# Performance work log

Hardware: AMD Instinct MI355X
Metric: run time of the kernel (lower is better)

Reference implementation:

```python
import jax, jax.numpy as jnp
import numpy as np

B, T, H = 1024, 256, 128

def _gru(x, Wx, Wh, b):
    # Keras GRU (reset_after=True), gate order z, r, h. x: [B,T,D], b: [2,3H]
    xp = x @ Wx + b[0]                      # [B,T,3H]
    h0 = jnp.zeros((x.shape[0], Wh.shape[0]), x.dtype)
    def step(h, xt):
        hp = h @ Wh + b[1]
        xz, xr, xh = jnp.split(xt, 3, axis=-1)
        hz, hr, hn = jnp.split(hp, 3, axis=-1)
        z = jax.nn.sigmoid(xz + hz)
        r = jax.nn.sigmoid(xr + hr)
        hh = jnp.tanh(xh + r * hn)
        return z * h + (1.0 - z) * hh, None
    h, _ = jax.lax.scan(step, h0, jnp.swapaxes(xp, 0, 1))
    return h                                 # [B,H]

def setup_inputs() -> dict:
    key = jax.random.key(0)
    ks = jax.random.split(key, 32)
    def gp(k, shape, scale=0.05):
        return (jax.random.normal(k, shape, dtype=jnp.float32) * scale)
    inp = {
        "spatial": jax.random.normal(ks[0], (B, T, 2), dtype=jnp.float32),
        "hour_idx": jax.random.randint(ks[1], (B, T), 0, 24, dtype=jnp.int32),
        "week_idx": jax.random.randint(ks[2], (B, T), 0, 7, dtype=jnp.int32),
        "E_time": gp(ks[3], (24, H)),
        "E_week": gp(ks[4], (7, H)),
        # spatial GRU (input dim 2)
        "Ws_x": gp(ks[5], (2, 3 * H)), "Ws_h": gp(ks[6], (H, 3 * H)), "bs": gp(ks[7], (2, 3 * H)),
        # hour temporal GRU (input dim 128)
        "Wh_x": gp(ks[8], (H, 3 * H)), "Wh_h": gp(ks[9], (H, 3 * H)), "bh": gp(ks[10], (2, 3 * H)),
        # week temporal GRU (input dim 128)
        "Ww_x": gp(ks[11], (H, 3 * H)), "Ww_h": gp(ks[12], (H, 3 * H)), "bw": gp(ks[13], (2, 3 * H)),
        # attention Dense(3) over the channel axis of size 3
        "Wa": gp(ks[14], (3, 3)), "ba": gp(ks[15], (3,)),
        # MLP
        "W1": gp(ks[16], (H, 1024)), "b1": gp(ks[17], (1024,)),
        "W2": gp(ks[18], (1024, 512)), "b2": gp(ks[19], (512,)),
        "W3": gp(ks[20], (512, 256)), "b3": gp(ks[21], (256,)),
        "W4": gp(ks[22], (256, H)), "b4": gp(ks[23], (H,)),
        "Wo": gp(ks[24], (H, 1)), "bo": gp(ks[25], (1,)),
    }
    return inp

def reference(spatial, hour_idx, week_idx, E_time, E_week,
              Ws_x, Ws_h, bs, Wh_x, Wh_h, bh, Ww_x, Ww_h, bw,
              Wa, ba, W1, b1, W2, b2, W3, b3, W4, b4, Wo, bo):
    te = E_time[hour_idx]                    # [B,T,128] gather
    we = E_week[week_idx]                    # [B,T,128] gather
    fs = _gru(spatial, Ws_x, Ws_h, bs)       # [B,128]
    fh = _gru(te, Wh_x, Wh_h, bh)            # [B,128]
    fw = _gru(we, Ww_x, Ww_h, bw)            # [B,128]
    allf = jnp.stack([fs, fh, fw], axis=-1)  # [B,128,3]
    scores = jax.nn.softmax(jax.nn.relu(allf @ Wa + ba), axis=-1)
    sf = jnp.sum(allf * scores, axis=-1)     # [B,128] attention-fused features
    x = jax.nn.relu(sf @ W1 + b1)
    x = jax.nn.relu(x @ W2 + b2)
    x = jax.nn.relu(x @ W3 + b3)
    x = jax.nn.relu(x @ W4 + b4)
    out = (x + sf) @ Wo + bo                 # residual then Dense(1)
    return out[:, 0]                         # [B]
```

## Files before the change

### kernel.cpp

```cpp
#include <hip/hip_runtime.h>
#include <hip/hip_bf16.h>

typedef __attribute__((ext_vector_type(8))) short short8;
typedef __attribute__((ext_vector_type(4))) float f32x4;
typedef __attribute__((ext_vector_type(2))) float f32x2;

#define LOG2E  1.44269504088896340736f
#define NLOG2E (-1.44269504088896340736f)
#define TLOG2E (2.88539008177792681472f)

#define HES 168

__device__ __forceinline__ unsigned short f2bf(float f) {
  unsigned u = __builtin_bit_cast(unsigned, f);
  u += 0x7fffu + ((u >> 16) & 1u);
  return (unsigned short)(u >> 16);
}

__global__ __launch_bounds__(256) void ptab_kernel(
    const float* __restrict__ E_time, const float* __restrict__ E_week,
    const float* __restrict__ Wh_x, const float* __restrict__ bh,
    const float* __restrict__ Ww_x, const float* __restrict__ bw,
    float* __restrict__ Ptime, float* __restrict__ Pweek)
{
  const int b = blockIdx.x;
  for (int c = threadIdx.x; c < 384; c += 256) {
    if (b < 24) {
      float acc = bh[c];
      for (int d = 0; d < 128; ++d)
        acc = fmaf(E_time[b * 128 + d], Wh_x[d * 384 + c], acc);
      Ptime[b * 384 + c] = acc;
    } else {
      const int r = b - 24;
      float acc = bw[c];
      for (int d = 0; d < 128; ++d)
        acc = fmaf(E_week[r * 128 + d], Ww_x[d * 384 + c], acc);
      Pweek[r * 384 + c] = acc;
    }
  }
}

__global__ __launch_bounds__(256, 1) void gru_kernel(
    const float* __restrict__ spatial,
    const int* __restrict__ hour_idx,
    const int* __restrict__ week_idx,
    const float* __restrict__ Ws_x,
    const float* __restrict__ Ws_h, const float* __restrict__ bs,
    const float* __restrict__ Wh_h, const float* __restrict__ bh,
    const float* __restrict__ Ww_h, const float* __restrict__ bw,
    const float* __restrict__ Ptime, const float* __restrict__ Pweek,
    const float* __restrict__ W1, const float* __restrict__ W2,
    const float* __restrict__ W3, const float* __restrict__ W4,
    unsigned short* __restrict__ Wt,
    float* __restrict__ fs, float* __restrict__ fh, float* __restrict__ fw)
{
  __shared__ __align__(16) unsigned short hx[2][16 * HES];
  __shared__ float ttile[64][65];

  const int tid = threadIdx.x;

  if (blockIdx.x >= 192) {
    const int tx = tid & 63, ty = tid >> 6;
    for (int t = blockIdx.x - 192; t < 200; t += 64) {
      const float* src; unsigned short* dst; int K, N, tk, tn; int tb = t;
      if (tb < 32)       { src = W1; dst = Wt;          K = 128;  N = 1024; tk = tb >> 4; tn = tb & 15; }
      else if (tb < 160) { tb -= 32;  src = W2; dst = Wt + 131072; K = 1024; N = 512;  tk = tb >> 3; tn = tb & 7; }
      else if (tb < 192) { tb -= 160; src = W3; dst = Wt + 655360; K = 512;  N = 256;  tk = tb >> 2; tn = tb & 3; }
      else               { tb -= 192; src = W4; dst = Wt + 786432; K = 256;  N = 128;  tk = tb >> 1; tn = tb & 1; }
      const int k0 = tk * 64, n0 = tn * 64;
      #pragma unroll
      for (int i = 0; i < 16; ++i)
        ttile[ty * 16 + i][tx] = src[(k0 + ty * 16 + i) * N + n0 + tx];
      __syncthreads();
      #pragma unroll
      for (int i = 0; i < 16; ++i)
        dst[(n0 + ty * 16 + i) * K + k0 + tx] = f2bf(ttile[tx][ty * 16 + i]);
      __syncthreads();
    }
    return;
  }

  const int lane = tid & 63;
  const int wv   = tid >> 6;
  const int ar   = lane & 15;
  const int akg  = lane >> 4;
  const int gid  = blockIdx.x;
  const int gru  = gid >> 6;
  const int row0 = (gid & 63) * 16;

  const float* __restrict__ Wh   = (gru == 0) ? Ws_h : (gru == 1) ? Wh_h : Ww_h;
  const float* __restrict__ bvec = (gru == 0) ? bs   : (gru == 1) ? bh   : bw;
  float* __restrict__ fout       = (gru == 0) ? fs   : (gru == 1) ? fh   : fw;
  const float* __restrict__ Ptab = (gru == 1) ? Ptime : Pweek;
  const int* __restrict__ idxg   = (gru == 1) ? hour_idx : week_idx;
  const int NR = (gru == 1) ? 24 : 7;

  const int jc[2] = {wv * 16 + ar, 64 + wv * 16 + ar};

  short8 wf[2][15];
  #pragma unroll
  for (int jh = 0; jh < 2; ++jh) {
    #pragma unroll
    for (int g = 0; g < 2; ++g) {
      #pragma unroll
      for (int ks = 0; ks < 5; ++ks) {
        short8 f;
        #pragma unroll
        for (int q = 0; q < 8; ++q) {
          const int k = ks * 32 + akg * 8 + q;
          const int col = g * 128 + jc[jh];
          float v;
          if (k < 128) v = Wh[k * 384 + col];
          else {
            const int p = k - 128;
            if (gru == 0) v = (p == 0) ? Ws_x[col] : (p == 1) ? Ws_x[384 + col] : 0.f;
            else          v = (p < NR) ? Ptab[p * 384 + col] : 0.f;
          }
          f[q] = (short)f2bf(v * NLOG2E);
        }
        wf[jh][g * 5 + ks] = f;
      }
    }
    #pragma unroll
    for (int ks = 0; ks < 4; ++ks) {
      short8 f;
      #pragma unroll
      for (int q = 0; q < 8; ++q) {
        const int k = ks * 32 + akg * 8 + q;
        f[q] = (short)f2bf(Wh[k * 384 + 256 + jc[jh]] * TLOG2E);
      }
      wf[jh][10 + ks] = f;
    }
    {
      short8 f;
      #pragma unroll
      for (int q = 0; q < 8; ++q) {
        const int p = akg * 8 + q;
        const int col = 256 + jc[jh];
        float v;
        if (gru == 0) v = (p == 0) ? Ws_x[col] : (p == 1) ? Ws_x[384 + col] : 0.f;
        else          v = (p < NR) ? Ptab[p * 384 + col] : 0.f;
        f[q] = (short)f2bf(v * TLOG2E);
      }
      wf[jh][14] = f;
    }
  }

  float bz[2], br[2], bnh[2], bnx[2];
  #pragma unroll
  for (int jh = 0; jh < 2; ++jh) {
    const int j = jc[jh];
    bz[jh]  = (bvec[384 + j]       + (gru == 0 ? bvec[j]       : 0.f)) * NLOG2E;
    br[jh]  = (bvec[384 + 128 + j] + (gru == 0 ? bvec[128 + j] : 0.f)) * NLOG2E;
    bnh[jh] = bvec[384 + 256 + j] * TLOG2E;
    bnx[jh] = (gru == 0 ? bvec[256 + j] : 0.f) * TLOG2E;
  }

  for (int e = tid; e < 2 * 16 * HES; e += 256) ((unsigned short*)hx)[e] = 0;
  __syncthreads();

  const bool mt  = (tid & 15) == 0;
  const int mrow = tid >> 4;
  f32x2 spn = {0.f, 0.f};
  int ix_prev = 0, ix_cur = 0, ix_next = 0;
  if (mt) {
    if (gru == 0) {
      const f32x2 s0 = *(const f32x2*)&spatial[(row0 + mrow) * 512];
      unsigned pk;
      asm("v_cvt_pk_bf16_f32 %0, %1, %2" : "=v"(pk) : "v"(s0.x), "v"(s0.y));
      *(unsigned*)&hx[0][mrow * HES + 128] = pk;
      spn = *(const f32x2*)&spatial[(row0 + mrow) * 512 + 2];
    } else {
      ix_cur = idxg[(row0 + mrow) * 256];
      hx[0][mrow * HES + 128 + ix_cur] = 0x3F80;
      ix_next = idxg[(row0 + mrow) * 256 + 1];
    }
  }
  __syncthreads();

  float hst[2][4];
  #pragma unroll
  for (int jh = 0; jh < 2; ++jh)
    #pragma unroll
    for (int q = 0; q < 4; ++q) hst[jh][q] = 0.f;

  const int abase = ar * HES;

  for (int t = 0; t < 256; ++t) {
    const unsigned short* __restrict__ hb = hx[t & 1];
    unsigned short* __restrict__ ho       = hx[(t + 1) & 1];

    short8 a[5];
    #pragma unroll
    for (int ks = 0; ks < 5; ++ks)
      a[ks] = *(const short8*)&hb[abase + ks * 32 + akg * 8];

    f32x2 msp = {0.f, 0.f};
    int ixn2 = 0;
    const bool mact = mt && (t + 1 < 256);
    if (mact && gru == 0 && t + 2 < 256)
      msp = *(const f32x2*)&spatial[(row0 + mrow) * 512 + 2 * (t + 2)];
    if (mact && gru != 0 && t + 2 < 256)
      ixn2 = idxg[(row0 + mrow) * 256 + t + 2];

    #pragma unroll
    for (int jh = 0; jh < 2; ++jh) {
      f32x4 az  = {bz[jh],  bz[jh],  bz[jh],  bz[jh]};
      f32x4 arr = {br[jh],  br[jh],  br[jh],  br[jh]};
      f32x4 anh = {bnh[jh], bnh[jh], bnh[jh], bnh[jh]};
      f32x4 anx = {bnx[jh], bnx[jh], bnx[jh], bnx[jh]};
      #pragma unroll
      for (int ks = 0; ks < 4; ++ks) {
        az  = __builtin_amdgcn_mfma_f32_16x16x32_bf16(a[ks], wf[jh][ks],      az,  0, 0, 0);
        arr = __builtin_amdgcn_mfma_f32_16x16x32_bf16(a[ks], wf[jh][5 + ks],  arr, 0, 0, 0);
        anh = __builtin_amdgcn_mfma_f32_16x16x32_bf16(a[ks], wf[jh][10 + ks], anh, 0, 0, 0);
      }
      az  = __builtin_amdgcn_mfma_f32_16x16x32_bf16(a[4], wf[jh][4],  az,  0, 0, 0);
      arr = __builtin_amdgcn_mfma_f32_16x16x32_bf16(a[4], wf[jh][9],  arr, 0, 0, 0);
      anx = __builtin_amdgcn_mfma_f32_16x16x32_bf16(a[4], wf[jh][14], anx, 0, 0, 0);

      float zg[4], rg[4], pz[4], pr[4];
      #pragma unroll
      for (int q = 0; q < 4; ++q) {
        pz[q] = 1.f + __builtin_amdgcn_exp2f(az[q]);
        pr[q] = 1.f + __builtin_amdgcn_exp2f(arr[q]);
      }
      #pragma unroll
      for (int p = 0; p < 4; p += 2) {
        const float A0 = pz[p] * pr[p];
        const float A1 = pz[p + 1] * pr[p + 1];
        const float inv = __builtin_amdgcn_rcpf(A0 * A1);
        const float t1 = A1 * inv, t0 = A0 * inv;
        zg[p]     = pr[p] * t1;     rg[p]     = pz[p] * t1;
        zg[p + 1] = pr[p + 1] * t0; rg[p + 1] = pz[p + 1] * t0;
      }
      float ph[4];
      #pragma unroll
      for (int q = 0; q < 4; ++q)
        ph[q] = 1.f + __builtin_amdgcn_exp2f(fmaf(rg[q], anh[q], anx[q]));
      float hn4[4];
      #pragma unroll
      for (int p = 0; p < 4; p += 2) {
        const float inv = __builtin_amdgcn_rcpf(ph[p] * ph[p + 1]);
        const float i0 = ph[p + 1] * inv;
        const float i1 = ph[p] * inv;
        const float hh0 = fmaf(-2.f, i0, 1.f);
        const float hh1 = fmaf(-2.f, i1, 1.f);
        hn4[p]     = fmaf(zg[p],     hst[jh][p]     - hh0, hh0);
        hn4[p + 1] = fmaf(zg[p + 1], hst[jh][p + 1] - hh1, hh1);
        hst[jh][p] = hn4[p]; hst[jh][p + 1] = hn4[p + 1];
      }

      unsigned p01, p23;
      asm("v_cvt_pk_bf16_f32 %0, %1, %2" : "=v"(p01) : "v"(hn4[0]), "v"(hn4[1]));
      asm("v_cvt_pk_bf16_f32 %0, %1, %2" : "=v"(p23) : "v"(hn4[2]), "v"(hn4[3]));
      const int j = jc[jh];
      ho[(akg * 4 + 0) * HES + j] = (unsigned short)(p01 & 0xffffu);
      ho[(akg * 4 + 1) * HES + j] = (unsigned short)(p01 >> 16);
      ho[(akg * 4 + 2) * HES + j] = (unsigned short)(p23 & 0xffffu);
      ho[(akg * 4 + 3) * HES + j] = (unsigned short)(p23 >> 16);
    }

    if (mact) {
      if (gru == 0) {
        unsigned pk;
        asm("v_cvt_pk_bf16_f32 %0, %1, %2" : "=v"(pk) : "v"(spn.x), "v"(spn.y));
        *(unsigned*)&ho[mrow * HES + 128] = pk;
        spn = msp;
      } else {
        if (t >= 1) ho[mrow * HES + 128 + ix_prev] = 0;
        ho[mrow * HES + 128 + ix_next] = 0x3F80;
        ix_prev = ix_cur; ix_cur = ix_next; ix_next = ixn2;
      }
    }

    __syncthreads();
  }

  #pragma unroll
  for (int jh = 0; jh < 2; ++jh)
    #pragma unroll
    for (int q = 0; q < 4; ++q)
      fout[(row0 + akg * 4 + q) * 128 + jc[jh]] = hst[jh][q];
}

template<int K, int N>
__device__ __forceinline__ void mlp_layer(
    const unsigned short* __restrict__ xin, unsigned short* __restrict__ xout,
    const unsigned short* __restrict__ Wt, const float* __restrict__ bias,
    int lane, int wv, float* __restrict__ foutF)
{
  constexpr int NT = N / 64;
  const int ar  = lane & 15;
  const int akg = lane >> 4;
  f32x4 acc[NT];
  #pragma unroll
  for (int nt = 0; nt < NT; ++nt) acc[nt] = f32x4{0.f, 0.f, 0.f, 0.f};
  for (int ks = 0; ks < K / 32; ++ks) {
    const short8 a = *(const short8*)&xin[ar * 1032 + ks * 32 + akg * 8];
    #pragma unroll
    for (int nt = 0; nt < NT; ++nt) {
      const int n = wv * (N / 4) + nt * 16 + ar;
      const short8 b = *(const short8*)&Wt[n * K + ks * 32 + akg * 8];
      acc[nt] = __builtin_amdgcn_mfma_f32_16x16x32_bf16(a, b, acc[nt], 0, 0, 0);
    }
  }
  const int rbase = akg * 4;
  #pragma unroll
  for (int nt = 0; nt < NT; ++nt) {
    const int n = wv * (N / 4) + nt * 16 + ar;
    const float bv = bias[n];
    #pragma unroll
    for (int q = 0; q < 4; ++q) {
      float v = acc[nt][q] + bv;
      v = fmaxf(v, 0.f);
      xout[(rbase + q) * 1032 + n] = f2bf(v);
      if (foutF) foutF[(rbase + q) * 128 + n] = v;
    }
  }
}

__global__ __launch_bounds__(256) void attn_mlp_kernel(
    const float* __restrict__ fs, const float* __restrict__ fh, const float* __restrict__ fw,
    const float* __restrict__ Wa, const float* __restrict__ ba,
    const unsigned short* __restrict__ Wt,
    const float* __restrict__ b1, const float* __restrict__ b2,
    const float* __restrict__ b3, const float* __restrict__ b4,
    const float* __restrict__ Wo, const float* __restrict__ bo,
    float* __restrict__ out)
{
  __shared__ __align__(16) unsigned short xa[16 * 1032];
  __shared__ __align__(16) unsigned short xb[16 * 1032];
  __shared__ __align__(16) float sf_l[16 * 128];
  __shared__ __align__(16) float x4f[16 * 128];

  const int tid  = threadIdx.x;
  const int lane = tid & 63;
  const int wv   = tid >> 6;
  const int row0 = blockIdx.x * 16;

  {
    const int i  = tid >> 4;
    const int j0 = (tid & 15) * 8;
    float wa[9], bav[3];
    #pragma unroll
    for (int q = 0; q < 9; ++q) wa[q] = Wa[q];
    #pragma unroll
    for (int q = 0; q < 3; ++q) bav[q] = ba[q];
    const int base = (row0 + i) * 128 + j0;
    #pragma unroll
    for (int half = 0; half < 2; ++half) {
      const f32x4 a = *(const f32x4*)&fs[base + half * 4];
      const f32x4 b = *(const f32x4*)&fh[base + half * 4];
      const f32x4 c = *(const f32x4*)&fw[base + half * 4];
      #pragma unroll
      for (int q = 0; q < 4; ++q) {
        const float f0 = a[q], f1 = b[q], f2 = c[q];
        float s0 = f0 * wa[0] + f1 * wa[3] + f2 * wa[6] + bav[0];
        float s1 = f0 * wa[1] + f1 * wa[4] + f2 * wa[7] + bav[1];
        float s2 = f0 * wa[2] + f1 * wa[5] + f2 * wa[8] + bav[2];
        s0 = fmaxf(s0, 0.f); s1 = fmaxf(s1, 0.f); s2 = fmaxf(s2, 0.f);
        const float m  = fmaxf(s0, fmaxf(s1, s2));
        const float e0 = __builtin_amdgcn_exp2f((s0 - m) * LOG2E);
        const float e1 = __builtin_amdgcn_exp2f((s1 - m) * LOG2E);
        const float e2 = __builtin_amdgcn_exp2f((s2 - m) * LOG2E);
        const float inv = __builtin_amdgcn_rcpf(e0 + e1 + e2);
        const float sf  = (f0 * e0 + f1 * e1 + f2 * e2) * inv;
        const int jj = j0 + half * 4 + q;
        sf_l[i * 128 + jj] = sf;
        xa[i * 1032 + jj]  = f2bf(sf);
      }
    }
  }
  __syncthreads();

  mlp_layer<128, 1024>(xa, xb, Wt,          b1, lane, wv, nullptr);
  __syncthreads();
  mlp_layer<1024, 512>(xb, xa, Wt + 131072, b2, lane, wv, nullptr);
  __syncthreads();
  mlp_layer<512,  256>(xa, xb, Wt + 655360, b3, lane, wv, nullptr);
  __syncthreads();
  mlp_layer<256,  128>(xb, xa, Wt + 786432, b4, lane, wv, x4f);
  __syncthreads();

  const int row = tid >> 4;
  const int p   = tid & 15;
  float part = 0.f;
  #pragma unroll
  for (int q = 0; q < 8; ++q) {
    const int jj = p + q * 16;
    part += (x4f[row * 128 + jj] + sf_l[row * 128 + jj]) * Wo[jj];
  }
  #pragma unroll
  for (int off = 8; off > 0; off >>= 1)
    part += __shfl_xor(part, off, 16);
  if (p == 0) out[row0 + row] = part + bo[0];
}

extern "C" void kernel_launch(void* const* d_in, const int* in_sizes, int n_in,
                              void* d_out, int out_size, void* d_ws, size_t ws_size,
                              hipStream_t stream) {
  const float* spatial  = (const float*)d_in[0];
  const int*   hour_idx = (const int*)d_in[1];
  const int*   week_idx = (const int*)d_in[2];
  const float* E_time   = (const float*)d_in[3];
  const float* E_week   = (const float*)d_in[4];
  const float* Ws_x = (const float*)d_in[5];
  const float* Ws_h = (const float*)d_in[6];
  const float* bs   = (const float*)d_in[7];
  const float* Wh_x = (const float*)d_in[8];
  const float* Wh_h = (const float*)d_in[9];
  const float* bh   = (const float*)d_in[10];
  const float* Ww_x = (const float*)d_in[11];
  const float* Ww_h = (const float*)d_in[12];
  const float* bw   = (const float*)d_in[13];
  const float* Wa   = (const float*)d_in[14];
  const float* ba   = (const float*)d_in[15];
  const float* W1   = (const float*)d_in[16];
  const float* b1   = (const float*)d_in[17];
  const float* W2   = (const float*)d_in[18];
  const float* b2   = (const float*)d_in[19];
  const float* W3   = (const float*)d_in[20];
  const float* b3   = (const float*)d_in[21];
  const float* W4   = (const float*)d_in[22];
  const float* b4   = (const float*)d_in[23];
  const float* Wo   = (const float*)d_in[24];
  const float* bo   = (const float*)d_in[25];
  float* out = (float*)d_out;

  float* ws    = (float*)d_ws;
  float* Ptime = ws;
  float* Pweek = Ptime + 9216;
  float* fsb   = Pweek + 2688;
  float* fhb   = fsb + 131072;
  float* fwb   = fhb + 131072;
  unsigned short* Wt = (unsigned short*)(fwb + 131072);

  ptab_kernel<<<31, 256, 0, stream>>>(E_time, E_week, Wh_x, bh, Ww_x, bw, Ptime, Pweek);
  gru_kernel<<<256, 256, 0, stream>>>(spatial, hour_idx, week_idx, Ws_x,
      Ws_h, bs, Wh_h, bh, Ww_h, bw, Ptime, Pweek,
      W1, W2, W3, W4, Wt, fsb, fhb, fwb);
  attn_mlp_kernel<<<64, 256, 0, stream>>>(fsb, fhb, fwb, Wa, ba, Wt,
      b1, b2, b3, b4, Wo, bo, out);
}
```

Baseline: 280.2 us.

## Pair two GRU chunks per block and ping-pong MFMA and gate phases

```diff
diff --git a/kernel.cpp b/kernel.cpp
--- a/kernel.cpp
+++ b/kernel.cpp
@@ -40,7 +40,7 @@
   }
 }
 
-__global__ __launch_bounds__(256, 1) void gru_kernel(
+__global__ __launch_bounds__(512, 2) void gru_kernel(
     const float* __restrict__ spatial,
     const int* __restrict__ hour_idx,
     const int* __restrict__ week_idx,
@@ -54,39 +54,40 @@
     unsigned short* __restrict__ Wt,
     float* __restrict__ fs, float* __restrict__ fh, float* __restrict__ fw)
 {
-  __shared__ __align__(16) unsigned short hx[2][16 * HES];
-  __shared__ float ttile[64][65];
+  __shared__ __align__(16) unsigned short smem[4][16 * HES];
 
   const int tid = threadIdx.x;
 
-  if (blockIdx.x >= 192) {
+  if (blockIdx.x >= 96) {
+    float (*ttile)[65] = (float (*)[65])smem;
+    int tb = blockIdx.x - 96;
+    const float* src; unsigned short* dst; int K, N, tk, tn;
+    if (tb < 32)       { src = W1; dst = Wt;          K = 128;  N = 1024; tk = tb >> 4; tn = tb & 15; }
+    else if (tb < 160) { tb -= 32;  src = W2; dst = Wt + 131072; K = 1024; N = 512;  tk = tb >> 3; tn = tb & 7; }
+    else if (tb < 192) { tb -= 160; src = W3; dst = Wt + 655360; K = 512;  N = 256;  tk = tb >> 2; tn = tb & 3; }
+    else               { tb -= 192; src = W4; dst = Wt + 786432; K = 256;  N = 128;  tk = tb >> 1; tn = tb & 1; }
     const int tx = tid & 63, ty = tid >> 6;
-    for (int t = blockIdx.x - 192; t < 200; t += 64) {
-      const float* src; unsigned short* dst; int K, N, tk, tn; int tb = t;
-      if (tb < 32)       { src = W1; dst = Wt;          K = 128;  N = 1024; tk = tb >> 4; tn = tb & 15; }
-      else if (tb < 160) { tb -= 32;  src = W2; dst = Wt + 131072; K = 1024; N = 512;  tk = tb >> 3; tn = tb & 7; }
-      else if (tb < 192) { tb -= 160; src = W3; dst = Wt + 655360; K = 512;  N = 256;  tk = tb >> 2; tn = tb & 3; }
-      else               { tb -= 192; src = W4; dst = Wt + 786432; K = 256;  N = 128;  tk = tb >> 1; tn = tb & 1; }
-      const int k0 = tk * 64, n0 = tn * 64;
-      #pragma unroll
-      for (int i = 0; i < 16; ++i)
-        ttile[ty * 16 + i][tx] = src[(k0 + ty * 16 + i) * N + n0 + tx];
-      __syncthreads();
-      #pragma unroll
-      for (int i = 0; i < 16; ++i)
-        dst[(n0 + ty * 16 + i) * K + k0 + tx] = f2bf(ttile[tx][ty * 16 + i]);
-      __syncthreads();
-    }
+    const int k0 = tk * 64, n0 = tn * 64;
+    #pragma unroll
+    for (int i = 0; i < 8; ++i)
+      ttile[ty * 8 + i][tx] = src[(k0 + ty * 8 + i) * N + n0 + tx];
+    __syncthreads();
+    #pragma unroll
+    for (int i = 0; i < 8; ++i)
+      dst[(n0 + ty * 8 + i) * K + k0 + tx] = f2bf(ttile[tx][ty * 8 + i]);
     return;
   }
 
   const int lane = tid & 63;
   const int wv   = tid >> 6;
+  const int ch   = wv >> 2;
+  const int wvc  = wv & 3;
   const int ar   = lane & 15;
   const int akg  = lane >> 4;
-  const int gid  = blockIdx.x;
-  const int gru  = gid >> 6;
-  const int row0 = (gid & 63) * 16;
+
+  const int chunk = blockIdx.x * 2 + ch;
+  const int gru   = chunk >> 6;
+  const int row0  = (chunk & 63) * 16;
 
   const float* __restrict__ Wh   = (gru == 0) ? Ws_h : (gru == 1) ? Wh_h : Ww_h;
   const float* __restrict__ bvec = (gru == 0) ? bs   : (gru == 1) ? bh   : bw;
@@ -95,7 +96,7 @@
   const int* __restrict__ idxg   = (gru == 1) ? hour_idx : week_idx;
   const int NR = (gru == 1) ? 24 : 7;
 
-  const int jc[2] = {wv * 16 + ar, 64 + wv * 16 + ar};
+  const int jc[2] = {wvc * 16 + ar, 64 + wvc * 16 + ar};
 
   short8 wf[2][15];
   #pragma unroll
@@ -156,11 +157,14 @@
     bnx[jh] = (gru == 0 ? bvec[256 + j] : 0.f) * TLOG2E;
   }
 
-  for (int e = tid; e < 2 * 16 * HES; e += 256) ((unsigned short*)hx)[e] = 0;
-  __syncthreads();
-
-  const bool mt  = (tid & 15) == 0;
-  const int mrow = tid >> 4;
+  unsigned short (*buf)[16 * HES] = &smem[ch * 2];
+
+  for (int e = wvc * 64 + lane; e < 2 * 16 * HES; e += 256)
+    ((unsigned short*)buf)[e] = 0;
+  __syncthreads();
+
+  const bool mt   = (ar == 0);
+  const int mrow  = wvc * 4 + akg;
   f32x2 spn = {0.f, 0.f};
   int ix_prev = 0, ix_cur = 0, ix_next = 0;
   if (mt) {
@@ -168,11 +172,11 @@
       const f32x2 s0 = *(const f32x2*)&spatial[(row0 + mrow) * 512];
       unsigned pk;
       asm("v_cvt_pk_bf16_f32 %0, %1, %2" : "=v"(pk) : "v"(s0.x), "v"(s0.y));
-      *(unsigned*)&hx[0][mrow * HES + 128] = pk;
+      *(unsigned*)&buf[0][mrow * HES + 128] = pk;
       spn = *(const f32x2*)&spatial[(row0 + mrow) * 512 + 2];
     } else {
       ix_cur = idxg[(row0 + mrow) * 256];
-      hx[0][mrow * HES + 128 + ix_cur] = 0x3F80;
+      buf[0][mrow * HES + 128 + ix_cur] = 0x3F80;
       ix_next = idxg[(row0 + mrow) * 256 + 1];
     }
   }
@@ -184,46 +188,42 @@
     #pragma unroll
     for (int q = 0; q < 4; ++q) hst[jh][q] = 0.f;
 
+  f32x4 az[2], arr[2], anh[2], anx[2];
   const int abase = ar * HES;
 
-  for (int t = 0; t < 256; ++t) {
-    const unsigned short* __restrict__ hb = hx[t & 1];
-    unsigned short* __restrict__ ho       = hx[(t + 1) & 1];
-
+  auto MPH = [&](int t) {
+    const unsigned short* __restrict__ hb = buf[t & 1];
     short8 a[5];
     #pragma unroll
     for (int ks = 0; ks < 5; ++ks)
       a[ks] = *(const short8*)&hb[abase + ks * 32 + akg * 8];
-
-    f32x2 msp = {0.f, 0.f};
-    int ixn2 = 0;
-    const bool mact = mt && (t + 1 < 256);
-    if (mact && gru == 0 && t + 2 < 256)
-      msp = *(const f32x2*)&spatial[(row0 + mrow) * 512 + 2 * (t + 2)];
-    if (mact && gru != 0 && t + 2 < 256)
-      ixn2 = idxg[(row0 + mrow) * 256 + t + 2];
-
     #pragma unroll
     for (int jh = 0; jh < 2; ++jh) {
-      f32x4 az  = {bz[jh],  bz[jh],  bz[jh],  bz[jh]};
-      f32x4 arr = {br[jh],  br[jh],  br[jh],  br[jh]};
-      f32x4 anh = {bnh[jh], bnh[jh], bnh[jh], bnh[jh]};
-      f32x4 anx = {bnx[jh], bnx[jh], bnx[jh], bnx[jh]};
+      az[jh]  = f32x4{bz[jh],  bz[jh],  bz[jh],  bz[jh]};
+      arr[jh] = f32x4{br[jh],  br[jh],  br[jh],  br[jh]};
+      anh[jh] = f32x4{bnh[jh], bnh[jh], bnh[jh], bnh[jh]};
+      anx[jh] = f32x4{bnx[jh], bnx[jh], bnx[jh], bnx[jh]};
       #pragma unroll
       for (int ks = 0; ks < 4; ++ks) {
-        az  = __builtin_amdgcn_mfma_f32_16x16x32_bf16(a[ks], wf[jh][ks],      az,  0, 0, 0);
-        arr = __builtin_amdgcn_mfma_f32_16x16x32_bf16(a[ks], wf[jh][5 + ks],  arr, 0, 0, 0);
-        anh = __builtin_amdgcn_mfma_f32_16x16x32_bf16(a[ks], wf[jh][10 + ks], anh, 0, 0, 0);
-      }
-      az  = __builtin_amdgcn_mfma_f32_16x16x32_bf16(a[4], wf[jh][4],  az,  0, 0, 0);
-      arr = __builtin_amdgcn_mfma_f32_16x16x32_bf16(a[4], wf[jh][9],  arr, 0, 0, 0);
-      anx = __builtin_amdgcn_mfma_f32_16x16x32_bf16(a[4], wf[jh][14], anx, 0, 0, 0);
-
+        az[jh]  = __builtin_amdgcn_mfma_f32_16x16x32_bf16(a[ks], wf[jh][ks],      az[jh],  0, 0, 0);
+        arr[jh] = __builtin_amdgcn_mfma_f32_16x16x32_bf16(a[ks], wf[jh][5 + ks],  arr[jh], 0, 0, 0);
+        anh[jh] = __builtin_amdgcn_mfma_f32_16x16x32_bf16(a[ks], wf[jh][10 + ks], anh[jh], 0, 0, 0);
+      }
+      az[jh]  = __builtin_amdgcn_mfma_f32_16x16x32_bf16(a[4], wf[jh][4],  az[jh],  0, 0, 0);
+      arr[jh] = __builtin_amdgcn_mfma_f32_16x16x32_bf16(a[4], wf[jh][9],  arr[jh], 0, 0, 0);
+      anx[jh] = __builtin_amdgcn_mfma_f32_16x16x32_bf16(a[4], wf[jh][14], anx[jh], 0, 0, 0);
+    }
+  };
+
+  auto GPH = [&](int t) {
+    unsigned short* __restrict__ ho = buf[(t + 1) & 1];
+    #pragma unroll
+    for (int jh = 0; jh < 2; ++jh) {
       float zg[4], rg[4], pz[4], pr[4];
       #pragma unroll
       for (int q = 0; q < 4; ++q) {
-        pz[q] = 1.f + __builtin_amdgcn_exp2f(az[q]);
-        pr[q] = 1.f + __builtin_amdgcn_exp2f(arr[q]);
+        pz[q] = 1.f + __builtin_amdgcn_exp2f(az[jh][q]);
+        pr[q] = 1.f + __builtin_amdgcn_exp2f(arr[jh][q]);
       }
       #pragma unroll
       for (int p = 0; p < 4; p += 2) {
@@ -237,7 +237,7 @@
       float ph[4];
       #pragma unroll
       for (int q = 0; q < 4; ++q)
-        ph[q] = 1.f + __builtin_amdgcn_exp2f(fmaf(rg[q], anh[q], anx[q]));
+        ph[q] = 1.f + __builtin_amdgcn_exp2f(fmaf(rg[q], anh[jh][q], anx[jh][q]));
       float hn4[4];
       #pragma unroll
       for (int p = 0; p < 4; p += 2) {
@@ -250,7 +250,6 @@
         hn4[p + 1] = fmaf(zg[p + 1], hst[jh][p + 1] - hh1, hh1);
         hst[jh][p] = hn4[p]; hst[jh][p + 1] = hn4[p + 1];
       }
-
       unsigned p01, p23;
       asm("v_cvt_pk_bf16_f32 %0, %1, %2" : "=v"(p01) : "v"(hn4[0]), "v"(hn4[1]));
       asm("v_cvt_pk_bf16_f32 %0, %1, %2" : "=v"(p23) : "v"(hn4[2]), "v"(hn4[3]));
@@ -260,20 +259,28 @@
       ho[(akg * 4 + 2) * HES + j] = (unsigned short)(p23 & 0xffffu);
       ho[(akg * 4 + 3) * HES + j] = (unsigned short)(p23 >> 16);
     }
-
-    if (mact) {
+    if (mt && t + 1 < 256) {
       if (gru == 0) {
         unsigned pk;
         asm("v_cvt_pk_bf16_f32 %0, %1, %2" : "=v"(pk) : "v"(spn.x), "v"(spn.y));
         *(unsigned*)&ho[mrow * HES + 128] = pk;
-        spn = msp;
+        if (t + 2 < 256) spn = *(const f32x2*)&spatial[(row0 + mrow) * 512 + 2 * (t + 2)];
       } else {
         if (t >= 1) ho[mrow * HES + 128 + ix_prev] = 0;
         ho[mrow * HES + 128 + ix_next] = 0x3F80;
-        ix_prev = ix_cur; ix_cur = ix_next; ix_next = ixn2;
-      }
-    }
-
+        ix_prev = ix_cur; ix_cur = ix_next;
+        if (t + 2 < 256) ix_next = idxg[(row0 + mrow) * 256 + t + 2];
+      }
+    }
+  };
+
+  for (int m = 0; m <= 256; ++m) {
+    if (ch == 0) { if (m < 256) MPH(m); }
+    else         { if (m >= 1)  GPH(m - 1); }
+    __syncthreads();
+    if (m == 256) break;
+    if (ch == 0) GPH(m);
+    else         MPH(m);
     __syncthreads();
   }
 
@@ -437,7 +444,7 @@
   unsigned short* Wt = (unsigned short*)(fwb + 131072);
 
   ptab_kernel<<<31, 256, 0, stream>>>(E_time, E_week, Wh_x, bh, Ww_x, bw, Ptime, Pweek);
-  gru_kernel<<<256, 256, 0, stream>>>(spatial, hour_idx, week_idx, Ws_x,
+  gru_kernel<<<296, 512, 0, stream>>>(spatial, hour_idx, week_idx, Ws_x,
       Ws_h, bs, Wh_h, bh, Ww_h, bw, Ptime, Pweek,
       W1, W2, W3, W4, Wt, fsb, fhb, fwb);
   attn_mlp_kernel<<<64, 256, 0, stream>>>(fsb, fhb, fwb, Wa, ba, Wt,
```

Measured after the change: 472.4 us. +68.6%, slower.
